# Performance work log

Hardware: AMD Instinct MI355X
Metric: run time of the kernel (lower is better)

Reference implementation:

```python
import jax, jax.numpy as jnp
import numpy as np

N, E = 50000, 800000
F_IN, HID, CLS, K = 128, 128, 40, 4


def setup_inputs() -> dict:
    key = jax.random.key(0)
    ks = jax.random.split(key, 6)
    x = jax.random.normal(ks[0], (N, F_IN), jnp.float32)
    edge_src = jax.random.randint(ks[1], (E,), 0, N, jnp.int32)
    edge_dst = jax.random.randint(ks[2], (E,), 0, N, jnp.int32)
    glorot = lambda k, sh, fan: jax.random.normal(k, sh, jnp.float32) * np.float32(1.0 / np.sqrt(fan))
    W0 = glorot(ks[3], (K, F_IN, HID), F_IN)
    W1 = glorot(ks[4], (K, HID, HID), HID)
    W2 = glorot(ks[5], (K, HID, CLS), HID)
    b0 = jnp.zeros((HID,), jnp.float32)
    b1 = jnp.zeros((HID,), jnp.float32)
    b2 = jnp.zeros((CLS,), jnp.float32)
    return dict(x=x, edge_src=edge_src, edge_dst=edge_dst,
                W0=W0, b0=b0, W1=W1, b1=b1, W2=W2, b2=b2)


def _cheb_edge_norm(edge_src, edge_dst, n):
    # PyG ChebConv 'sym' norm with lambda_max=2: scaled Laplacian
    # L_hat = 2L/lambda_max - I = -D^{-1/2} A D^{-1/2}  (diagonal is exactly 0)
    ones = jnp.ones(edge_src.shape[0], jnp.float32)
    deg = jax.ops.segment_sum(ones, edge_src, num_segments=n)
    dinv = jnp.where(deg > 0, jax.lax.rsqrt(jnp.maximum(deg, 1.0)), 0.0)
    return -dinv[edge_src] * dinv[edge_dst]  # [E]


def _cheb_conv(x, edge_src, edge_dst, w_norm, W, b, n):
    # Chebyshev recurrence: Tx0 = x, Tx1 = L_hat x, Tx_k = 2 L_hat Tx_{k-1} - Tx_{k-2}
    def lhat(t):  # SpMM: out[dst] += w * t[src]
        return jax.ops.segment_sum(t[edge_src] * w_norm[:, None], edge_dst, num_segments=n)

    Tx0 = x
    out = Tx0 @ W[0]
    Tx1 = lhat(Tx0)
    out = out + Tx1 @ W[1]
    for k in range(2, W.shape[0]):
        Tx2 = 2.0 * lhat(Tx1) - Tx0
        out = out + Tx2 @ W[k]
        Tx0, Tx1 = Tx1, Tx2
    return out + b


def reference(x, edge_src, edge_dst, W0, b0, W1, b1, W2, b2):
    n = x.shape[0]
    w_norm = _cheb_edge_norm(edge_src, edge_dst, n)
    h = x
    x1 = h
    for W, b in ((W0, b0), (W1, b1), (W2, b2)):
        x1 = _cheb_conv(h, edge_src, edge_dst, w_norm, W, b, n)
        h = jax.nn.relu(x1)  # dropout(p=0.6) is identity in eval mode
    # original returns log_softmax of the LAST conv's pre-activation x1
    return jax.nn.log_softmax(x1, axis=1)
```

## Files before the change

### kernel.cpp

```cpp
#include <hip/hip_runtime.h>
#include <math.h>

#define NN 50000
#define NE 800000
#define FDIM 128
#define CLS 40
#define AW 512
#define ZW 256
#define RSLOT 64

typedef __attribute__((ext_vector_type(8))) short short8v;
typedef __attribute__((ext_vector_type(8))) unsigned short ushort8v;
typedef __attribute__((ext_vector_type(4))) float f32x4;

__device__ inline float b2f(unsigned short u) {
    union { unsigned int i; float f; } v; v.i = ((unsigned)u) << 16; return v.f;
}
__device__ inline unsigned short f2b(float f) {
    unsigned int x = __float_as_uint(f);
    unsigned int r = (x + 0x7fffu + ((x >> 16) & 1u)) >> 16;
    return (unsigned short)r;
}


#define NB_Z0 196
#define NB_Z1 782

__global__ __launch_bounds__(256) void zero_k(int* degi, int* fill, int4* ews4) {
    int b = blockIdx.x;
    if (b < NB_Z0) {
        int i = b * 256 + threadIdx.x;
        if (i < NN) { degi[i] = 0; fill[i] = 0; }
    } else {
        int base = (b - NB_Z0) * 1024;
        int4 v = make_int4(NN, NN, NN, NN);
        #pragma unroll
        for (int j = 0; j < 4; j++) {
            int idx = base + j * 256 + threadIdx.x;
            if (idx < NN * RSLOT / 4) ews4[idx] = v;
        }
    }
}

#define NB_ES   782
#define NB_CVT  3125
#define NB_WH   256
#define NB_WZ   128

__global__ __launch_bounds__(256) void prep_k(
        const int4* __restrict__ esrc4, const int4* __restrict__ edst4,
        int* degi, int* fill, int* __restrict__ ews,
        const float* __restrict__ x, unsigned short* __restrict__ Ab,
        const float* __restrict__ W0, const float* __restrict__ W1,
        const float* __restrict__ W2,
        unsigned short* __restrict__ Wt0, unsigned short* __restrict__ Wt1,
        unsigned short* __restrict__ Wz) {
    int b = blockIdx.x;
    int tid = threadIdx.x;
    if (b < NB_ES) {
        int e = b * 256 + tid;
        if (e < NE / 4) {
            int4 s = esrc4[e], d = edst4[e];
            atomicAdd(&degi[s.x], 1); atomicAdd(&degi[s.y], 1);
            atomicAdd(&degi[s.z], 1); atomicAdd(&degi[s.w], 1);
            int c0 = atomicAdd(&fill[d.x], 1);
            int c1 = atomicAdd(&fill[d.y], 1);
            int c2 = atomicAdd(&fill[d.z], 1);
            int c3 = atomicAdd(&fill[d.w], 1);
            if (c0 < RSLOT) ews[d.x * RSLOT + c0] = s.x;
            if (c1 < RSLOT) ews[d.y * RSLOT + c1] = s.y;
            if (c2 < RSLOT) ews[d.z * RSLOT + c2] = s.z;
            if (c3 < RSLOT) ews[d.w * RSLOT + c3] = s.w;
        }
    } else if (b < NB_ES + NB_CVT) {
        int i = (b - NB_ES) * 256 + tid;
        int row = i >> 4, cg = i & 15;
        const float4* xp = (const float4*)(x + (size_t)row * FDIM + cg * 8);
        float4 v0 = xp[0], v1 = xp[1];
        ushort8v r;
        r[0] = f2b(v0.x); r[1] = f2b(v0.y); r[2] = f2b(v0.z); r[3] = f2b(v0.w);
        r[4] = f2b(v1.x); r[5] = f2b(v1.y); r[6] = f2b(v1.z); r[7] = f2b(v1.w);
        *(ushort8v*)(Ab + (size_t)row * AW + cg * 8) = r;
    } else if (b < NB_ES + NB_CVT + 2 * NB_WH) {
        int wi = b - NB_ES - NB_CVT;
        const float* W = (wi < NB_WH) ? W0 : W1;
        unsigned short* Wfm = (wi < NB_WH) ? Wt0 : Wt1;
        int i = (wi % NB_WH) * 256 + tid;
        int j = i & 7, l = (i >> 3) & 63, kcl = (i >> 9) & 3, nt = (i >> 11) & 7, c = i >> 14;
        int r = kcl * 32 + (l >> 4) * 8 + j;
        int col = nt * 16 + (l & 15);
        Wfm[i] = f2b(W[((size_t)c * 128 + r) * 128 + col]);
    } else {
        int i = (b - NB_ES - NB_CVT - 2 * NB_WH) * 256 + tid;
        int j = i & 7, l = (i >> 3) & 63, kcl = (i >> 9) & 3, nt = (i >> 11) & 7, half = (i >> 14) & 1;
        int k = kcl * 32 + (l >> 4) * 8 + j;
        int col = half * 128 + nt * 16 + (l & 15);
        int kcheb = col >> 6, cc = col & 63;
        float v = (cc < CLS) ? W2[((size_t)kcheb * 128 + k) * CLS + cc] : 0.0f;
        Wz[i] = f2b(v);
    }
}

__global__ void dinv_k(const int* __restrict__ degi, float* __restrict__ dinv) {
    int i = blockIdx.x * blockDim.x + threadIdx.x;
    if (i < NN) {
        int d = degi[i];
        dinv[i] = (d > 0) ? rsqrtf((float)d) : 0.0f;
    } else if (i == NN) {
        dinv[i] = 0.0f;
    }
}


template <bool CHEB>
__global__ __launch_bounds__(256) void spmm_k(const unsigned short* __restrict__ inp,
                                              const unsigned short* __restrict__ prevp,
                                              unsigned short* __restrict__ outp,
                                              const int* __restrict__ fill,
                                              const int* __restrict__ ews,
                                              const float* __restrict__ dinv) {
    int row = blockIdx.x * 4 + (threadIdx.x >> 6);
    int lane = threadIdx.x & 63;
    int slot = lane >> 4, ln = lane & 15;
    int n = fill[row];
    if (n > RSLOT) n = RSLOT;
    int nr = (n + 15) & ~15;
    int e0 = row * RSLOT;
    float dvr = dinv[row];
    float acc[8] = {0.f, 0.f, 0.f, 0.f, 0.f, 0.f, 0.f, 0.f};
    for (int e = e0; e < e0 + nr; e += 16) {
        int4 s4 = *(const int4*)&ews[e + slot * 4];
        ushort8v t0 = *(const ushort8v*)(inp + (size_t)s4.x * AW + ln * 8);
        ushort8v t1 = *(const ushort8v*)(inp + (size_t)s4.y * AW + ln * 8);
        ushort8v t2 = *(const ushort8v*)(inp + (size_t)s4.z * AW + ln * 8);
        ushort8v t3 = *(const ushort8v*)(inp + (size_t)s4.w * AW + ln * 8);
        float w0 = -dinv[s4.x] * dvr, w1 = -dinv[s4.y] * dvr;
        float w2 = -dinv[s4.z] * dvr, w3 = -dinv[s4.w] * dvr;
        #pragma unroll
        for (int j = 0; j < 8; j++)
            acc[j] += w0 * b2f(t0[j]) + w1 * b2f(t1[j]) + w2 * b2f(t2[j]) + w3 * b2f(t3[j]);
    }
    #pragma unroll
    for (int j = 0; j < 8; j++) {
        acc[j] += __shfl_xor(acc[j], 16);
        acc[j] += __shfl_xor(acc[j], 32);
    }
    if (slot == 0) {
        ushort8v r;
        if (CHEB) {
            ushort8v p = *(const ushort8v*)(prevp + (size_t)row * AW + ln * 8);
            #pragma unroll
            for (int j = 0; j < 8; j++) r[j] = f2b(2.f * acc[j] - b2f(p[j]));
        } else {
            #pragma unroll
            for (int j = 0; j < 8; j++) r[j] = f2b(acc[j]);
        }
        *(ushort8v*)(outp + (size_t)row * AW + ln * 8) = r;
    }
}


template <int MODE>
__global__ __launch_bounds__(256) void spmm64_k(const unsigned short* __restrict__ gsrc,
                                                const unsigned short* __restrict__ zadd,
                                                const unsigned short* __restrict__ bsub,
                                                unsigned short* __restrict__ wout,
                                                float* __restrict__ fout,
                                                const int* __restrict__ fill,
                                                const int* __restrict__ ews,
                                                const float* __restrict__ dinv) {
    constexpr int GS = (MODE == 0) ? ZW : 64;
    constexpr float SC = (MODE == 2) ? 1.0f : 2.0f;
    int row = blockIdx.x * 4 + (threadIdx.x >> 6);
    int lane = threadIdx.x & 63;
    int slot = lane >> 3, ln = lane & 7;
    int n = fill[row];
    if (n > RSLOT) n = RSLOT;
    int nr = (n + 31) & ~31;
    int e0 = row * RSLOT;
    float dvr = dinv[row];
    float acc[8] = {0.f, 0.f, 0.f, 0.f, 0.f, 0.f, 0.f, 0.f};
    for (int e = e0; e < e0 + nr; e += 32) {
        int4 s4 = *(const int4*)&ews[e + slot * 4];
        ushort8v t0 = *(const ushort8v*)(gsrc + (size_t)s4.x * GS + ln * 8);
        ushort8v t1 = *(const ushort8v*)(gsrc + (size_t)s4.y * GS + ln * 8);
        ushort8v t2 = *(const ushort8v*)(gsrc + (size_t)s4.z * GS + ln * 8);
        ushort8v t3 = *(const ushort8v*)(gsrc + (size_t)s4.w * GS + ln * 8);
        float w0 = -dinv[s4.x] * dvr, w1 = -dinv[s4.y] * dvr;
        float w2 = -dinv[s4.z] * dvr, w3 = -dinv[s4.w] * dvr;
        #pragma unroll
        for (int j = 0; j < 8; j++)
            acc[j] += w0 * b2f(t0[j]) + w1 * b2f(t1[j]) + w2 * b2f(t2[j]) + w3 * b2f(t3[j]);
    }
    #pragma unroll
    for (int j = 0; j < 8; j++) {
        acc[j] += __shfl_xor(acc[j], 8);
        acc[j] += __shfl_xor(acc[j], 16);
        acc[j] += __shfl_xor(acc[j], 32);
    }
    if (slot != 0) return;
    ushort8v zv = *(const ushort8v*)(zadd + (size_t)row * ZW + ln * 8);
    float v[8];
    if (MODE == 0) {
        #pragma unroll
        for (int j = 0; j < 8; j++) v[j] = b2f(zv[j]) + SC * acc[j];
    } else {
        constexpr int BS = (MODE == 1) ? ZW : 64;
        ushort8v bv = *(const ushort8v*)(bsub + (size_t)row * BS + ln * 8);
        #pragma unroll
        for (int j = 0; j < 8; j++) v[j] = b2f(zv[j]) + SC * acc[j] - b2f(bv[j]);
    }
    if (MODE < 2) {
        ushort8v r;
        #pragma unroll
        for (int j = 0; j < 8; j++) r[j] = f2b(v[j]);
        *(ushort8v*)(wout + (size_t)row * 64 + ln * 8) = r;
    } else {
        float m = -INFINITY;
        #pragma unroll
        for (int j = 0; j < 8; j++) if (ln * 8 + j < CLS) m = fmaxf(m, v[j]);
        #pragma unroll
        for (int off = 4; off >= 1; off >>= 1) m = fmaxf(m, __shfl_xor(m, off));
        float s = 0.f;
        #pragma unroll
        for (int j = 0; j < 8; j++) if (ln * 8 + j < CLS) s += __expf(v[j] - m);
        #pragma unroll
        for (int off = 4; off >= 1; off >>= 1) s += __shfl_xor(s, off);
        float ls = logf(s) + m;
        #pragma unroll
        for (int j = 0; j < 8; j++) {
            int col = ln * 8 + j;
            if (col < CLS) fout[(size_t)row * CLS + col] = v[j] - ls;
        }
    }
}


__global__ __launch_bounds__(256) void gemm_hid_k(const unsigned short* __restrict__ A,
                                                  const unsigned short* __restrict__ Wfm,
                                                  const float* __restrict__ bias,
                                                  unsigned short* __restrict__ Hout) {
    __shared__ unsigned short Blds[16384];
    int tid = threadIdx.x;
    int w = tid >> 6, lane = tid & 63, ln = lane & 15, gp = lane >> 4;
    int rowbase = blockIdx.x * 64 + w * 16;
    int rowc = rowbase + ln;
    if (rowc >= NN) rowc = NN - 1;
    const unsigned short* Arow = A + (size_t)rowc * AW + gp * 8;

    f32x4 acc[8];
    #pragma unroll
    for (int i = 0; i < 8; i++) acc[i] = (f32x4){0.f, 0.f, 0.f, 0.f};

    short8v acur[4], anxt[4];
    #pragma unroll
    for (int kcl = 0; kcl < 4; kcl++) acur[kcl] = *(const short8v*)(Arow + kcl * 32);
    {
        const ushort8v* g = (const ushort8v*)Wfm;
        ushort8v* s = (ushort8v*)Blds;
        #pragma unroll
        for (int i = 0; i < 8; i++) s[tid + i * 256] = g[tid + i * 256];
    }
    __syncthreads();

    for (int c = 0; c < 4; c++) {
        if (c < 3) {
            #pragma unroll
            for (int kcl = 0; kcl < 4; kcl++)
                anxt[kcl] = *(const short8v*)(Arow + (c + 1) * 128 + kcl * 32);
        }
        #pragma unroll
        for (int kcl = 0; kcl < 4; kcl++) {
            #pragma unroll
            for (int nt = 0; nt < 8; nt++) {
                short8v b = *(const short8v*)&Blds[((nt * 4 + kcl) * 64 + lane) * 8];
                acc[nt] = __builtin_amdgcn_mfma_f32_16x16x32_bf16(acur[kcl], b, acc[nt], 0, 0, 0);
            }
        }
        if (c < 3) {
            __syncthreads();
            const ushort8v* g = (const ushort8v*)(Wfm + (c + 1) * 16384);
            ushort8v* s = (ushort8v*)Blds;
            #pragma unroll
            for (int i = 0; i < 8; i++) s[tid + i * 256] = g[tid + i * 256];
            __syncthreads();
            #pragma unroll
            for (int kcl = 0; kcl < 4; kcl++) acur[kcl] = anxt[kcl];
        }
    }

    if (rowbase < NN) {
        #pragma unroll
        for (int nt = 0; nt < 8; nt++) {
            int col = nt * 16 + ln;
            float bv = bias[col];
            #pragma unroll
            for (int j = 0; j < 4; j++) {
                int r = rowbase + gp * 4 + j;
                Hout[(size_t)r * AW + col] = f2b(fmaxf(acc[nt][j] + bv, 0.0f));
            }
        }
    }
}


__global__ __launch_bounds__(256) void gemm_z_k(const unsigned short* __restrict__ A,
                                                const unsigned short* __restrict__ Wz,
                                                const float* __restrict__ b2,
                                                unsigned short* __restrict__ Z) {
    __shared__ unsigned short Blds[16384];
    int tid = threadIdx.x;
    int w = tid >> 6, lane = tid & 63, ln = lane & 15, gp = lane >> 4;
    int rowbase = blockIdx.x * 64 + w * 16;
    int rowc = rowbase + ln;
    if (rowc >= NN) rowc = NN - 1;
    const unsigned short* Arow = A + (size_t)rowc * AW + gp * 8;

    short8v af[4];
    #pragma unroll
    for (int kcl = 0; kcl < 4; kcl++) af[kcl] = *(const short8v*)(Arow + kcl * 32);

    for (int half = 0; half < 2; half++) {
        if (half) __syncthreads();
        {
            const ushort8v* g = (const ushort8v*)(Wz + half * 16384);
            ushort8v* s = (ushort8v*)Blds;
            #pragma unroll
            for (int i = 0; i < 8; i++) s[tid + i * 256] = g[tid + i * 256];
        }
        __syncthreads();
        f32x4 acc[8];
        #pragma unroll
        for (int i = 0; i < 8; i++) acc[i] = (f32x4){0.f, 0.f, 0.f, 0.f};
        #pragma unroll
        for (int kcl = 0; kcl < 4; kcl++) {
            #pragma unroll
            for (int nt = 0; nt < 8; nt++) {
                short8v b = *(const short8v*)&Blds[((nt * 4 + kcl) * 64 + lane) * 8];
                acc[nt] = __builtin_amdgcn_mfma_f32_16x16x32_bf16(af[kcl], b, acc[nt], 0, 0, 0);
            }
        }
        if (rowbase < NN) {
            #pragma unroll
            for (int nt = 0; nt < 8; nt++) {
                int col = half * 128 + nt * 16 + ln;
                float bv = (col < CLS) ? b2[col] : 0.0f;
                #pragma unroll
                for (int j = 0; j < 4; j++) {
                    int r = rowbase + gp * 4 + j;
                    Z[(size_t)r * ZW + col] = f2b(acc[nt][j] + bv);
                }
            }
        }
    }
}


extern "C" void kernel_launch(void* const* d_in, const int* in_sizes, int n_in,
                              void* d_out, int out_size, void* d_ws, size_t ws_size,
                              hipStream_t stream) {
    const float* x    = (const float*)d_in[0];
    const int*   esrc = (const int*)d_in[1];
    const int*   edst = (const int*)d_in[2];
    const float* W0   = (const float*)d_in[3];
    const float* b0   = (const float*)d_in[4];
    const float* W1   = (const float*)d_in[5];
    const float* b1   = (const float*)d_in[6];
    const float* W2   = (const float*)d_in[7];
    const float* b2   = (const float*)d_in[8];
    float* out = (float*)d_out;

    char* p = (char*)d_ws;
    auto alloc = [&](size_t bytes) -> void* {
        void* r = (void*)p;
        p += (bytes + 255) & ~(size_t)255;
        return r;
    };
    unsigned short* Abuf = (unsigned short*)alloc((size_t)(NN + 1) * AW * 2);
    unsigned short* Zbuf = (unsigned short*)alloc((size_t)(NN + 1) * ZW * 2);
    unsigned short* B1b  = (unsigned short*)alloc((size_t)(NN + 1) * 64 * 2);
    unsigned short* B2b  = (unsigned short*)alloc((size_t)(NN + 1) * 64 * 2);
    int*   ews  = (int*)alloc((size_t)NN * RSLOT * 4);
    unsigned short* Wt0  = (unsigned short*)alloc((size_t)128 * AW * 2);
    unsigned short* Wt1  = (unsigned short*)alloc((size_t)128 * AW * 2);
    unsigned short* Wz   = (unsigned short*)alloc((size_t)32768 * 2);
    int*   degi = (int*)alloc(NN * 4);
    int*   fill = (int*)alloc(NN * 4);
    float* dinv = (float*)alloc((NN + 1) * 4);

    const int TB = 256;
    int gN1 = (NN + 1 + TB - 1) / TB;

    zero_k<<<NB_Z0 + NB_Z1, TB, 0, stream>>>(degi, fill, (int4*)ews);
    prep_k<<<NB_ES + NB_CVT + 2 * NB_WH + NB_WZ, TB, 0, stream>>>(
        (const int4*)esrc, (const int4*)edst, degi, fill, ews,
        x, Abuf, W0, W1, W2, Wt0, Wt1, Wz);
    dinv_k<<<gN1, TB, 0, stream>>>(degi, dinv);

    int gSpmm = (NN + 3) / 4;
    int gGemm = (NN + 63) / 64;

    unsigned short* s0 = Abuf + 0 * 128;
    unsigned short* s1 = Abuf + 1 * 128;
    unsigned short* s2 = Abuf + 2 * 128;
    unsigned short* s3 = Abuf + 3 * 128;

    for (int l = 0; l < 2; l++) {
        spmm_k<false><<<gSpmm, TB, 0, stream>>>(s0, nullptr, s1, fill, ews, dinv);
        spmm_k<true><<<gSpmm, TB, 0, stream>>>(s1, s0, s2, fill, ews, dinv);
        spmm_k<true><<<gSpmm, TB, 0, stream>>>(s2, s1, s3, fill, ews, dinv);
        const unsigned short* Wt = (l == 0) ? Wt0 : Wt1;
        const float* bl = (l == 0) ? b0 : b1;
        gemm_hid_k<<<gGemm, TB, 0, stream>>>(Abuf, Wt, bl, Abuf);
    }

    gemm_z_k<<<gGemm, TB, 0, stream>>>(Abuf, Wz, b2, Zbuf);
    spmm64_k<0><<<gSpmm, TB, 0, stream>>>(Zbuf + 192, Zbuf + 128, nullptr,
                                          B2b, nullptr, fill, ews, dinv);
    spmm64_k<1><<<gSpmm, TB, 0, stream>>>(B2b, Zbuf + 64, Zbuf + 192,
                                          B1b, nullptr, fill, ews, dinv);
    spmm64_k<2><<<gSpmm, TB, 0, stream>>>(B1b, Zbuf, B2b,
                                          nullptr, out, fill, ews, dinv);
}
```

Baseline: 396.2 us.

## Build exact CSR via bucketed counting sort instead of fixed-slot padded adjacency

Replaces the padded 64-slot-per-row adjacency, which was filled with global atomics and initialised with a large zeroing pass, by a real CSR built from a per-block histogram over destination buckets, a three-kernel prefix scan, a partition pass and an in-bucket counting sort. SpMM kernels now walk exact row-pointer ranges with aligned vector loads, masking out-of-range slots to a dummy node. This removes the 12.8MB zero fill and the padded gathers, and drops the old silent truncation of rows with more than 64 edges. In exchange it adds several small launches and a serial single-thread scan in scanB_k.

```diff
diff --git a/kernel.cpp b/kernel.cpp
--- a/kernel.cpp
+++ b/kernel.cpp
@@ -7,7 +7,16 @@
 #define CLS 40
 #define AW 512
 #define ZW 256
-#define RSLOT 64
+
+#define BSH 7
+#define BINS 128
+#define NBUK 391
+#define NB_E 196
+#define EUNITS 1024
+#define U4 (NE / 4)
+#define HL (NBUK * NB_E)
+#define SCAN_CHUNK 2048
+#define NB_S ((HL + SCAN_CHUNK - 1) / SCAN_CHUNK)
 
 typedef __attribute__((ext_vector_type(8))) short short8v;
 typedef __attribute__((ext_vector_type(8))) unsigned short ushort8v;
@@ -22,34 +31,13 @@
     return (unsigned short)r;
 }
 
-
-#define NB_Z0 196
-#define NB_Z1 782
-
-__global__ __launch_bounds__(256) void zero_k(int* degi, int* fill, int4* ews4) {
-    int b = blockIdx.x;
-    if (b < NB_Z0) {
-        int i = b * 256 + threadIdx.x;
-        if (i < NN) { degi[i] = 0; fill[i] = 0; }
-    } else {
-        int base = (b - NB_Z0) * 1024;
-        int4 v = make_int4(NN, NN, NN, NN);
-        #pragma unroll
-        for (int j = 0; j < 4; j++) {
-            int idx = base + j * 256 + threadIdx.x;
-            if (idx < NN * RSLOT / 4) ews4[idx] = v;
-        }
-    }
-}
-
-#define NB_ES   782
 #define NB_CVT  3125
 #define NB_WH   256
 #define NB_WZ   128
 
 __global__ __launch_bounds__(256) void prep_k(
         const int4* __restrict__ esrc4, const int4* __restrict__ edst4,
-        int* degi, int* fill, int* __restrict__ ews,
+        int* degi, int* __restrict__ hist,
         const float* __restrict__ x, unsigned short* __restrict__ Ab,
         const float* __restrict__ W0, const float* __restrict__ W1,
         const float* __restrict__ W2,
@@ -57,23 +45,25 @@
         unsigned short* __restrict__ Wz) {
     int b = blockIdx.x;
     int tid = threadIdx.x;
-    if (b < NB_ES) {
-        int e = b * 256 + tid;
-        if (e < NE / 4) {
-            int4 s = esrc4[e], d = edst4[e];
-            atomicAdd(&degi[s.x], 1); atomicAdd(&degi[s.y], 1);
-            atomicAdd(&degi[s.z], 1); atomicAdd(&degi[s.w], 1);
-            int c0 = atomicAdd(&fill[d.x], 1);
-            int c1 = atomicAdd(&fill[d.y], 1);
-            int c2 = atomicAdd(&fill[d.z], 1);
-            int c3 = atomicAdd(&fill[d.w], 1);
-            if (c0 < RSLOT) ews[d.x * RSLOT + c0] = s.x;
-            if (c1 < RSLOT) ews[d.y * RSLOT + c1] = s.y;
-            if (c2 < RSLOT) ews[d.z * RSLOT + c2] = s.z;
-            if (c3 < RSLOT) ews[d.w * RSLOT + c3] = s.w;
-        }
-    } else if (b < NB_ES + NB_CVT) {
-        int i = (b - NB_ES) * 256 + tid;
+    if (b < NB_E) {
+        __shared__ int lcnt[NBUK];
+        for (int i = tid; i < NBUK; i += 256) lcnt[i] = 0;
+        __syncthreads();
+        #pragma unroll
+        for (int it = 0; it < 4; it++) {
+            int u = b * EUNITS + it * 256 + tid;
+            if (u < U4) {
+                int4 s = esrc4[u], d = edst4[u];
+                atomicAdd(&degi[s.x], 1); atomicAdd(&degi[s.y], 1);
+                atomicAdd(&degi[s.z], 1); atomicAdd(&degi[s.w], 1);
+                atomicAdd(&lcnt[d.x >> BSH], 1); atomicAdd(&lcnt[d.y >> BSH], 1);
+                atomicAdd(&lcnt[d.z >> BSH], 1); atomicAdd(&lcnt[d.w >> BSH], 1);
+            }
+        }
+        __syncthreads();
+        for (int i = tid; i < NBUK; i += 256) hist[i * NB_E + b] = lcnt[i];
+    } else if (b < NB_E + NB_CVT) {
+        int i = (b - NB_E) * 256 + tid;
         int row = i >> 4, cg = i & 15;
         const float4* xp = (const float4*)(x + (size_t)row * FDIM + cg * 8);
         float4 v0 = xp[0], v1 = xp[1];
@@ -81,8 +71,8 @@
         r[0] = f2b(v0.x); r[1] = f2b(v0.y); r[2] = f2b(v0.z); r[3] = f2b(v0.w);
         r[4] = f2b(v1.x); r[5] = f2b(v1.y); r[6] = f2b(v1.z); r[7] = f2b(v1.w);
         *(ushort8v*)(Ab + (size_t)row * AW + cg * 8) = r;
-    } else if (b < NB_ES + NB_CVT + 2 * NB_WH) {
-        int wi = b - NB_ES - NB_CVT;
+    } else if (b < NB_E + NB_CVT + 2 * NB_WH) {
+        int wi = b - NB_E - NB_CVT;
         const float* W = (wi < NB_WH) ? W0 : W1;
         unsigned short* Wfm = (wi < NB_WH) ? Wt0 : Wt1;
         int i = (wi % NB_WH) * 256 + tid;
@@ -91,7 +81,7 @@
         int col = nt * 16 + (l & 15);
         Wfm[i] = f2b(W[((size_t)c * 128 + r) * 128 + col]);
     } else {
-        int i = (b - NB_ES - NB_CVT - 2 * NB_WH) * 256 + tid;
+        int i = (b - NB_E - NB_CVT - 2 * NB_WH) * 256 + tid;
         int j = i & 7, l = (i >> 3) & 63, kcl = (i >> 9) & 3, nt = (i >> 11) & 7, half = (i >> 14) & 1;
         int k = kcl * 32 + (l >> 4) * 8 + j;
         int col = half * 128 + nt * 16 + (l & 15);
@@ -101,13 +91,134 @@
     }
 }
 
-__global__ void dinv_k(const int* __restrict__ degi, float* __restrict__ dinv) {
+
+__global__ void scanA_k(const int* __restrict__ hist, int* __restrict__ bsum) {
+    __shared__ int lds[256];
+    int base = blockIdx.x * SCAN_CHUNK;
+    int s = 0;
+    for (int j = threadIdx.x; j < SCAN_CHUNK; j += 256) {
+        int i = base + j;
+        if (i < HL) s += hist[i];
+    }
+    lds[threadIdx.x] = s;
+    __syncthreads();
+    for (int off = 128; off > 0; off >>= 1) {
+        if (threadIdx.x < off) lds[threadIdx.x] += lds[threadIdx.x + off];
+        __syncthreads();
+    }
+    if (threadIdx.x == 0) bsum[blockIdx.x] = lds[0];
+}
+
+__global__ void scanB_k(int* bsum, int* scanned) {
+    if (threadIdx.x == 0 && blockIdx.x == 0) {
+        int run = 0;
+        for (int b = 0; b < NB_S; b++) { int t = bsum[b]; bsum[b] = run; run += t; }
+        scanned[HL] = run;
+    }
+}
+
+__global__ void scanC_k(const int* __restrict__ hist, const int* __restrict__ bsum,
+                        int* __restrict__ scanned) {
+    __shared__ int lds[256];
+    int base = blockIdx.x * SCAN_CHUNK + threadIdx.x * 8;
+    int v[8];
+    int s = 0;
+    #pragma unroll
+    for (int j = 0; j < 8; j++) {
+        int i = base + j;
+        v[j] = (i < HL) ? hist[i] : 0;
+        s += v[j];
+    }
+    lds[threadIdx.x] = s;
+    __syncthreads();
+    for (int off = 1; off < 256; off <<= 1) {
+        int t = (threadIdx.x >= (unsigned)off) ? lds[threadIdx.x - off] : 0;
+        __syncthreads();
+        lds[threadIdx.x] += t;
+        __syncthreads();
+    }
+    int incl = lds[threadIdx.x];
+    int excl = incl - s;
+    int run = bsum[blockIdx.x] + excl;
+    #pragma unroll
+    for (int j = 0; j < 8; j++) {
+        int i = base + j;
+        if (i < HL) scanned[i] = run;
+        run += v[j];
+    }
+}
+
+
+__global__ __launch_bounds__(256) void part_k(const int4* __restrict__ esrc4,
+                                              const int4* __restrict__ edst4,
+                                              const int* __restrict__ scanned,
+                                              int* __restrict__ ebuf) {
+    __shared__ int lcnt[NBUK];
+    int b = blockIdx.x;
+    int tid = threadIdx.x;
+    for (int i = tid; i < NBUK; i += 256) lcnt[i] = 0;
+    __syncthreads();
+    #pragma unroll
+    for (int it = 0; it < 4; it++) {
+        int u = b * EUNITS + it * 256 + tid;
+        if (u < U4) {
+            int4 s = esrc4[u], d = edst4[u];
+            int dd[4] = {d.x, d.y, d.z, d.w};
+            int ss[4] = {s.x, s.y, s.z, s.w};
+            #pragma unroll
+            for (int j = 0; j < 4; j++) {
+                int bin = dd[j] >> BSH;
+                int r = atomicAdd(&lcnt[bin], 1);
+                int pos = scanned[bin * NB_E + b] + r;
+                ebuf[pos] = ((dd[j] & (BINS - 1)) << 16) | ss[j];
+            }
+        }
+    }
+}
+
+
+__global__ __launch_bounds__(256) void bsort_k(const int* __restrict__ scanned,
+                                               const int* __restrict__ ebuf,
+                                               int* __restrict__ ews,
+                                               int* __restrict__ rp) {
+    __shared__ int cnt[BINS], excl[BINS], rnk[BINS];
+    int b = blockIdx.x;
+    int tid = threadIdx.x;
+    int s0b = scanned[b * NB_E];
+    int s1b = scanned[(b + 1) * NB_E];
+    if (tid < BINS) { cnt[tid] = 0; rnk[tid] = 0; }
+    __syncthreads();
+    for (int e = s0b + tid; e < s1b; e += 256)
+        atomicAdd(&cnt[ebuf[e] >> 16], 1);
+    __syncthreads();
+    if (tid == 0) {
+        int run = 0;
+        for (int i = 0; i < BINS; i++) { excl[i] = run; run += cnt[i]; }
+    }
+    __syncthreads();
+    if (tid < BINS) {
+        int node = b * BINS + tid;
+        if (node <= NN) rp[node] = s0b + excl[tid];
+    }
+    for (int e = s0b + tid; e < s1b; e += 256) {
+        int pk = ebuf[e];
+        int low = pk >> 16;
+        int pos = s0b + excl[low] + atomicAdd(&rnk[low], 1);
+        ews[pos] = pk & 0xFFFF;
+    }
+}
+
+
+__global__ void dinv_k(const int* __restrict__ degi, float* __restrict__ dinv,
+                       int* __restrict__ ews) {
     int i = blockIdx.x * blockDim.x + threadIdx.x;
     if (i < NN) {
         int d = degi[i];
         dinv[i] = (d > 0) ? rsqrtf((float)d) : 0.0f;
     } else if (i == NN) {
         dinv[i] = 0.0f;
+    } else if (i <= NN + 32) {
+        ews[NE + (i - NN - 1)] = NN;
     }
 }
 
@@ -116,26 +227,29 @@
 __global__ __launch_bounds__(256) void spmm_k(const unsigned short* __restrict__ inp,
                                               const unsigned short* __restrict__ prevp,
                                               unsigned short* __restrict__ outp,
-                                              const int* __restrict__ fill,
+                                              const int* __restrict__ rp,
                                               const int* __restrict__ ews,
                                               const float* __restrict__ dinv) {
     int row = blockIdx.x * 4 + (threadIdx.x >> 6);
     int lane = threadIdx.x & 63;
     int slot = lane >> 4, ln = lane & 15;
-    int n = fill[row];
-    if (n > RSLOT) n = RSLOT;
-    int nr = (n + 15) & ~15;
-    int e0 = row * RSLOT;
+    int e0 = rp[row], e1 = rp[row + 1];
+    int eb = e0 & ~15;
     float dvr = dinv[row];
     float acc[8] = {0.f, 0.f, 0.f, 0.f, 0.f, 0.f, 0.f, 0.f};
-    for (int e = e0; e < e0 + nr; e += 16) {
-        int4 s4 = *(const int4*)&ews[e + slot * 4];
-        ushort8v t0 = *(const ushort8v*)(inp + (size_t)s4.x * AW + ln * 8);
-        ushort8v t1 = *(const ushort8v*)(inp + (size_t)s4.y * AW + ln * 8);
-        ushort8v t2 = *(const ushort8v*)(inp + (size_t)s4.z * AW + ln * 8);
-        ushort8v t3 = *(const ushort8v*)(inp + (size_t)s4.w * AW + ln * 8);
-        float w0 = -dinv[s4.x] * dvr, w1 = -dinv[s4.y] * dvr;
-        float w2 = -dinv[s4.z] * dvr, w3 = -dinv[s4.w] * dvr;
+    for (int e = eb; e < e1; e += 16) {
+        int ee = e + slot * 4;
+        int4 s4 = *(const int4*)&ews[ee];
+        int sx = (ee     >= e0 && ee     < e1) ? s4.x : NN;
+        int sy = (ee + 1 >= e0 && ee + 1 < e1) ? s4.y : NN;
+        int sz = (ee + 2 >= e0 && ee + 2 < e1) ? s4.z : NN;
+        int sw = (ee + 3 >= e0 && ee + 3 < e1) ? s4.w : NN;
+        ushort8v t0 = *(const ushort8v*)(inp + (size_t)sx * AW + ln * 8);
+        ushort8v t1 = *(const ushort8v*)(inp + (size_t)sy * AW + ln * 8);
+        ushort8v t2 = *(const ushort8v*)(inp + (size_t)sz * AW + ln * 8);
+        ushort8v t3 = *(const ushort8v*)(inp + (size_t)sw * AW + ln * 8);
+        float w0 = -dinv[sx] * dvr, w1 = -dinv[sy] * dvr;
+        float w2 = -dinv[sz] * dvr, w3 = -dinv[sw] * dvr;
         #pragma unroll
         for (int j = 0; j < 8; j++)
             acc[j] += w0 * b2f(t0[j]) + w1 * b2f(t1[j]) + w2 * b2f(t2[j]) + w3 * b2f(t3[j]);
@@ -166,7 +280,7 @@
                                                 const unsigned short* __restrict__ bsub,
                                                 unsigned short* __restrict__ wout,
                                                 float* __restrict__ fout,
-                                                const int* __restrict__ fill,
+                                                const int* __restrict__ rp,
                                                 const int* __restrict__ ews,
                                                 const float* __restrict__ dinv) {
     constexpr int GS = (MODE == 0) ? ZW : 64;
@@ -174,20 +288,23 @@
     int row = blockIdx.x * 4 + (threadIdx.x >> 6);
     int lane = threadIdx.x & 63;
     int slot = lane >> 3, ln = lane & 7;
-    int n = fill[row];
-    if (n > RSLOT) n = RSLOT;
-    int nr = (n + 31) & ~31;
-    int e0 = row * RSLOT;
+    int e0 = rp[row], e1 = rp[row + 1];
+    int eb = e0 & ~31;
     float dvr = dinv[row];
     float acc[8] = {0.f, 0.f, 0.f, 0.f, 0.f, 0.f, 0.f, 0.f};
-    for (int e = e0; e < e0 + nr; e += 32) {
-        int4 s4 = *(const int4*)&ews[e + slot * 4];
-        ushort8v t0 = *(const ushort8v*)(gsrc + (size_t)s4.x * GS + ln * 8);
-        ushort8v t1 = *(const ushort8v*)(gsrc + (size_t)s4.y * GS + ln * 8);
-        ushort8v t2 = *(const ushort8v*)(gsrc + (size_t)s4.z * GS + ln * 8);
-        ushort8v t3 = *(const ushort8v*)(gsrc + (size_t)s4.w * GS + ln * 8);
-        float w0 = -dinv[s4.x] * dvr, w1 = -dinv[s4.y] * dvr;
-        float w2 = -dinv[s4.z] * dvr, w3 = -dinv[s4.w] * dvr;
+    for (int e = eb; e < e1; e += 32) {
+        int ee = e + slot * 4;
+        int4 s4 = *(const int4*)&ews[ee];
+        int sx = (ee     >= e0 && ee     < e1) ? s4.x : NN;
+        int sy = (ee + 1 >= e0 && ee + 1 < e1) ? s4.y : NN;
+        int sz = (ee + 2 >= e0 && ee + 2 < e1) ? s4.z : NN;
+        int sw = (ee + 3 >= e0 && ee + 3 < e1) ? s4.w : NN;
+        ushort8v t0 = *(const ushort8v*)(gsrc + (size_t)sx * GS + ln * 8);
+        ushort8v t1 = *(const ushort8v*)(gsrc + (size_t)sy * GS + ln * 8);
+        ushort8v t2 = *(const ushort8v*)(gsrc + (size_t)sz * GS + ln * 8);
+        ushort8v t3 = *(const ushort8v*)(gsrc + (size_t)sw * GS + ln * 8);
+        float w0 = -dinv[sx] * dvr, w1 = -dinv[sy] * dvr;
+        float w2 = -dinv[sz] * dvr, w3 = -dinv[sw] * dvr;
         #pragma unroll
         for (int j = 0; j < 8; j++)
             acc[j] += w0 * b2f(t0[j]) + w1 * b2f(t1[j]) + w2 * b2f(t2[j]) + w3 * b2f(t3[j]);
@@ -380,22 +497,30 @@
     unsigned short* Zbuf = (unsigned short*)alloc((size_t)(NN + 1) * ZW * 2);
     unsigned short* B1b  = (unsigned short*)alloc((size_t)(NN + 1) * 64 * 2);
     unsigned short* B2b  = (unsigned short*)alloc((size_t)(NN + 1) * 64 * 2);
-    int*   ews  = (int*)alloc((size_t)NN * RSLOT * 4);
-    unsigned short* Wt0  = (unsigned short*)alloc((size_t)128 * AW * 2);
-    unsigned short* Wt1  = (unsigned short*)alloc((size_t)128 * AW * 2);
-    unsigned short* Wz   = (unsigned short*)alloc((size_t)32768 * 2);
+    int*   ews     = (int*)alloc((size_t)(NE + 32) * 4);
+    int*   ebuf    = (int*)alloc((size_t)NE * 4);
+    int*   hist    = (int*)alloc((size_t)HL * 4);
+    int*   scanned = (int*)alloc((size_t)(HL + 1) * 4);
+    int*   bsum    = (int*)alloc(NB_S * 4);
+    unsigned short* Wt0 = (unsigned short*)alloc((size_t)128 * AW * 2);
+    unsigned short* Wt1 = (unsigned short*)alloc((size_t)128 * AW * 2);
+    unsigned short* Wz  = (unsigned short*)alloc((size_t)32768 * 2);
     int*   degi = (int*)alloc(NN * 4);
-    int*   fill = (int*)alloc(NN * 4);
+    int*   rp   = (int*)alloc((NN + 1) * 4);
     float* dinv = (float*)alloc((NN + 1) * 4);
 
     const int TB = 256;
-    int gN1 = (NN + 1 + TB - 1) / TB;
-
-    zero_k<<<NB_Z0 + NB_Z1, TB, 0, stream>>>(degi, fill, (int4*)ews);
-    prep_k<<<NB_ES + NB_CVT + 2 * NB_WH + NB_WZ, TB, 0, stream>>>(
-        (const int4*)esrc, (const int4*)edst, degi, fill, ews,
+
+    hipMemsetAsync(degi, 0, NN * 4, stream);
+    prep_k<<<NB_E + NB_CVT + 2 * NB_WH + NB_WZ, TB, 0, stream>>>(
+        (const int4*)esrc, (const int4*)edst, degi, hist,
         x, Abuf, W0, W1, W2, Wt0, Wt1, Wz);
-    dinv_k<<<gN1, TB, 0, stream>>>(degi, dinv);
+    scanA_k<<<NB_S, TB, 0, stream>>>(hist, bsum);
+    scanB_k<<<1, 64, 0, stream>>>(bsum, scanned);
+    scanC_k<<<NB_S, TB, 0, stream>>>(hist, bsum, scanned);
+    part_k<<<NB_E, TB, 0, stream>>>((const int4*)esrc, (const int4*)edst, scanned, ebuf);
+    bsort_k<<<NBUK, TB, 0, stream>>>(scanned, ebuf, ews, rp);
+    dinv_k<<<(NN + 33 + TB - 1) / TB, TB, 0, stream>>>(degi, dinv, ews);
 
     int gSpmm = (NN + 3) / 4;
     int gGemm = (NN + 63) / 64;
@@ -406,9 +531,9 @@
     unsigned short* s3 = Abuf + 3 * 128;
 
     for (int l = 0; l < 2; l++) {
-        spmm_k<false><<<gSpmm, TB, 0, stream>>>(s0, nullptr, s1, fill, ews, dinv);
-        spmm_k<true><<<gSpmm, TB, 0, stream>>>(s1, s0, s2, fill, ews, dinv);
-        spmm_k<true><<<gSpmm, TB, 0, stream>>>(s2, s1, s3, fill, ews, dinv);
+        spmm_k<false><<<gSpmm, TB, 0, stream>>>(s0, nullptr, s1, rp, ews, dinv);
+        spmm_k<true><<<gSpmm, TB, 0, stream>>>(s1, s0, s2, rp, ews, dinv);
+        spmm_k<true><<<gSpmm, TB, 0, stream>>>(s2, s1, s3, rp, ews, dinv);
         const unsigned short* Wt = (l == 0) ? Wt0 : Wt1;
         const float* bl = (l == 0) ? b0 : b1;
         gemm_hid_k<<<gGemm, TB, 0, stream>>>(Abuf, Wt, bl, Abuf);
@@ -416,9 +541,9 @@
 
     gemm_z_k<<<gGemm, TB, 0, stream>>>(Abuf, Wz, b2, Zbuf);
     spmm64_k<0><<<gSpmm, TB, 0, stream>>>(Zbuf + 192, Zbuf + 128, nullptr,
-                                          B2b, nullptr, fill, ews, dinv);
+                                          B2b, nullptr, rp, ews, dinv);
     spmm64_k<1><<<gSpmm, TB, 0, stream>>>(B2b, Zbuf + 64, Zbuf + 192,
-                                          B1b, nullptr, fill, ews, dinv);
+                                          B1b, nullptr, rp, ews, dinv);
     spmm64_k<2><<<gSpmm, TB, 0, stream>>>(B1b, Zbuf, B2b,
-                                          nullptr, out, fill, ews, dinv);
-}
+                                          nullptr, out, rp, ews, dinv);
+}
```

Result: slower. 407.1 us (+2.7%).
